# Kernel optimization log

Hardware: AMD Instinct MI355X
Metric: run time of the kernel (lower is better)

## Reference

```python
import jax, jax.numpy as jnp
import numpy as np

EPS = 1e-5

def _bn(x, gamma, beta):
    # x: [B, N, C]; training-mode BatchNorm1d over (B, N)
    mu = jnp.mean(x, axis=(0, 1))
    var = jnp.var(x, axis=(0, 1))
    return (x - mu) * jax.lax.rsqrt(var + EPS) * gamma + beta


def setup_inputs() -> dict:
    key = jax.random.key(0)
    ks = jax.random.split(key, 32)
    B, N = 16, 8192
    enc_dim, mem_dim = 1024, 1024
    feat_dim = enc_dim + mem_dim  # 2048
    n_points = 2048
    s = 0.02
    d = {
        'partial': jax.random.normal(ks[0], (B, N, 3), jnp.float32),
        # first_conv: Conv1d(3,128,1) + BN(128) + ReLU + Conv1d(128,256,1)
        'W1': jax.random.normal(ks[1], (128, 3), jnp.float32) * s,
        'b1': jnp.zeros((128,), jnp.float32),
        'g1': jnp.ones((128,), jnp.float32),
        'be1': jnp.zeros((128,), jnp.float32),
        'W2': jax.random.normal(ks[2], (256, 128), jnp.float32) * s,
        'b2': jnp.zeros((256,), jnp.float32),
        # second_conv: Conv1d(512,512,1) + BN(512) + ReLU + Conv1d(512,enc_dim,1)
        'W3': jax.random.normal(ks[3], (512, 512), jnp.float32) * s,
        'b3': jnp.zeros((512,), jnp.float32),
        'g2': jnp.ones((512,), jnp.float32),
        'be2': jnp.zeros((512,), jnp.float32),
        'W4': jax.random.normal(ks[4], (enc_dim, 512), jnp.float32) * s,
        'b4': jnp.zeros((enc_dim,), jnp.float32),
        # MemoryModule gates: Linear(enc_dim, mem_dim) x4 + memory param
        'Wf': jax.random.normal(ks[5], (mem_dim, enc_dim), jnp.float32) * s,
        'bf': jnp.zeros((mem_dim,), jnp.float32),
        'Wi': jax.random.normal(ks[6], (mem_dim, enc_dim), jnp.float32) * s,
        'bi': jnp.zeros((mem_dim,), jnp.float32),
        'Wo': jax.random.normal(ks[7], (mem_dim, enc_dim), jnp.float32) * s,
        'bo': jnp.zeros((mem_dim,), jnp.float32),
        'Wc': jax.random.normal(ks[8], (mem_dim, enc_dim), jnp.float32) * s,
        'bc': jnp.zeros((mem_dim,), jnp.float32),
        'mem': jax.random.normal(ks[9], (1, mem_dim), jnp.float32),
        # Decoder MLP: feat_dim->2048->2048->2048->3*n_points
        'D1w': jax.random.normal(ks[10], (2048, feat_dim), jnp.float32) * s,
        'D1b': jnp.zeros((2048,), jnp.float32),
        'D2w': jax.random.normal(ks[11], (2048, 2048), jnp.float32) * s,
        'D2b': jnp.zeros((2048,), jnp.float32),
        'D3w': jax.random.normal(ks[12], (2048, 2048), jnp.float32) * s,
        'D3b': jnp.zeros((2048,), jnp.float32),
        'D4w': jax.random.normal(ks[13], (3 * n_points, 2048), jnp.float32) * s,
        'D4b': jnp.zeros((3 * n_points,), jnp.float32),
    }
    return d


def reference(partial, W1, b1, g1, be1, W2, b2, W3, b3, g2, be2, W4, b4,
              Wf, bf, Wi, bi, Wo, bo, Wc, bc, mem,
              D1w, D1b, D2w, D2b, D3w, D3b, D4w, D4b):
    B, N, _ = partial.shape
    # --- Encoder first_conv (pointwise convs == per-point linear) ---
    f = jnp.einsum('bnc,dc->bnd', partial, W1) + b1          # [B,N,128]
    f = jax.nn.relu(_bn(f, g1, be1))
    f = jnp.einsum('bnc,dc->bnd', f, W2) + b2                # [B,N,256]
    fg = jnp.max(f, axis=1, keepdims=True)                   # [B,1,256]
    f = jnp.concatenate([jnp.broadcast_to(fg, (B, N, 256)), f], axis=-1)  # [B,N,512]
    # --- second_conv ---
    f = jnp.einsum('bnc,dc->bnd', f, W3) + b3                # [B,N,512]
    f = jax.nn.relu(_bn(f, g2, be2))
    f = jnp.einsum('bnc,dc->bnd', f, W4) + b4                # [B,N,enc_dim]
    feat_global = jnp.max(f, axis=1)                         # [B,enc_dim]
    # --- MemoryModule (flag=False: memory not updated) ---
    fgate = jax.nn.sigmoid(feat_global @ Wf.T + bf)
    igate = jax.nn.sigmoid(feat_global @ Wi.T + bi)
    ogate = jax.nn.sigmoid(feat_global @ Wo.T + bo)
    cand = jnp.tanh(feat_global @ Wc.T + bc)
    mem_b = jnp.broadcast_to(mem, fgate.shape)
    h = ogate * jnp.tanh(fgate * mem_b + igate * cand)       # [B,mem_dim]
    feat = jnp.concatenate([feat_global, h], axis=1)         # [B,feat_dim]
    # --- Decoder MLP ---
    z = jax.nn.relu(feat @ D1w.T + D1b)
    z = jax.nn.relu(z @ D2w.T + D2b)
    z = jax.nn.relu(z @ D3w.T + D3b)
    z = z @ D4w.T + D4b                                      # [B, 3*n_points]
    return z.reshape(B, -1, 3)
```

## Files before the change

kernel.cpp:

```cpp
#include <hip/hip_runtime.h>
#include <hip/hip_bf16.h>

typedef __bf16 v8bf __attribute__((ext_vector_type(8)));
typedef float  v4f  __attribute__((ext_vector_type(4)));

#define NPTS (16*8192)
#define RPB  8192

__device__ __forceinline__ unsigned fenc(float x){
    unsigned u = __float_as_uint(x);
    return (u & 0x80000000u) ? ~u : (u | 0x80000000u);
}
__device__ __forceinline__ float fdec(unsigned u){
    return __uint_as_float((u & 0x80000000u) ? (u ^ 0x80000000u) : ~u);
}

__device__ __forceinline__ v8bf bn_relu8(v8bf v, float4 s0, float4 s1, float4 h0, float4 h1){
    v8bf r;
    r[0] = (__bf16)fmaxf(fmaf((float)v[0], s0.x, h0.x), 0.f);
    r[1] = (__bf16)fmaxf(fmaf((float)v[1], s0.y, h0.y), 0.f);
    r[2] = (__bf16)fmaxf(fmaf((float)v[2], s0.z, h0.z), 0.f);
    r[3] = (__bf16)fmaxf(fmaf((float)v[3], s0.w, h0.w), 0.f);
    r[4] = (__bf16)fmaxf(fmaf((float)v[4], s1.x, h1.x), 0.f);
    r[5] = (__bf16)fmaxf(fmaf((float)v[5], s1.y, h1.y), 0.f);
    r[6] = (__bf16)fmaxf(fmaf((float)v[6], s1.z, h1.z), 0.f);
    r[7] = (__bf16)fmaxf(fmaf((float)v[7], s1.w, h1.w), 0.f);
    return r;
}

__global__ __launch_bounds__(256) void stats1_k(const float* __restrict__ P,
        const float* __restrict__ W1, const float* __restrict__ b1,
        float* __restrict__ gsum, float* __restrict__ gsumsq)
{
    int tid = threadIdx.x;
    int c = tid & 127, half = tid >> 7;
    float w0 = W1[c*3+0], w1 = W1[c*3+1], w2 = W1[c*3+2], bb = b1[c];
    float s = 0.f, s2 = 0.f;
    int base = blockIdx.x * 512 + half;
    for (int i = 0; i < 256; ++i) {
        int p = base + i*2;
        float x = P[p*3+0], y = P[p*3+1], z = P[p*3+2];
        float v = fmaf(w0,x, fmaf(w1,y, fmaf(w2,z, bb)));
        s += v; s2 = fmaf(v,v,s2);
    }
    __shared__ float ls[256], lq[256];
    ls[tid] = s; lq[tid] = s2;
    __syncthreads();
    if (half == 0) {
        atomicAdd(&gsum[c],   s  + ls[tid+128]);
        atomicAdd(&gsumsq[c], s2 + lq[tid+128]);
    }
}

__global__ void finalize_k(const float* __restrict__ gsum, const float* __restrict__ gsumsq,
        const float* __restrict__ gamma, const float* __restrict__ beta,
        float* __restrict__ scale, float* __restrict__ shift, int C, float invn)
{
    int c = blockIdx.x*blockDim.x + threadIdx.x;
    if (c >= C) return;
    float m   = gsum[c]*invn;
    float var = fmaxf(gsumsq[c]*invn - m*m, 0.f);
    float rs  = rsqrtf(var + 1e-5f);
    float sc  = gamma[c]*rs;
    scale[c] = sc;
    shift[c] = beta[c] - m*sc;
}

__global__ __launch_bounds__(256) void apply1_k(const float* __restrict__ P,
        const float* __restrict__ W1, const float* __restrict__ b1,
        const float* __restrict__ sc, const float* __restrict__ sh,
        __bf16* __restrict__ out)
{
    int tid = threadIdx.x;
    int c = tid & 127, ph = tid >> 7;
    float w0 = W1[c*3+0], w1 = W1[c*3+1], w2 = W1[c*3+2], bb = b1[c];
    float a = sc[c], b_ = sh[c];
    int base = blockIdx.x * 16 + ph;
    #pragma unroll
    for (int i = 0; i < 8; ++i) {
        int p = base + i*2;
        float x = P[p*3+0], y = P[p*3+1], z = P[p*3+2];
        float v = fmaf(w0,x, fmaf(w1,y, fmaf(w2,z, bb)));
        v = fmaxf(fmaf(v, a, b_), 0.f);
        out[(size_t)p*128 + c] = (__bf16)v;
    }
}

__global__ void cvt_k(const float* __restrict__ src, __bf16* __restrict__ dst,
                      int rows, int cols, int sstride, int coff)
{
    int i = blockIdx.x*256 + threadIdx.x;
    if (i >= rows*cols) return;
    int r = i / cols, c = i - r*cols;
    dst[i] = (__bf16)src[(size_t)r*sstride + coff + c];
}

template<bool STORE, bool DOMAX, bool STATS, bool BNA, int LOGNB>
__global__ __launch_bounds__(256, 2) void gemm_k(
        const __bf16* __restrict__ A, const __bf16* __restrict__ Bw,
        int K, int Nw,
        const float* __restrict__ bias, int bias_bstride,
        __bf16* __restrict__ Cout, unsigned* __restrict__ maxenc,
        float* __restrict__ gsum, float* __restrict__ gsq,
        const float* __restrict__ scA, const float* __restrict__ shA)
{
    __shared__ __bf16 As[128*64];
    __shared__ __bf16 Bs[256*64];
    __shared__ float lstat[2][2][256];

    const int tid  = threadIdx.x;
    const int lane = tid & 63;
    const int wave = tid >> 6;
    const int wr = wave >> 1, wc = wave & 1;
    const int nwg   = (int)gridDim.x;
    const int chunk = nwg >> 3;
    const int bi    = (int)blockIdx.x;
    const int li    = (bi & 7) * chunk + (bi >> 3);
    const int m0    = (li >> LOGNB) * 128;
    const int n0    = (li & ((1 << LOGNB) - 1)) * 256;
    const int srow = tid >> 3, sslot = tid & 7;

    v4f acc[4][8];
    #pragma unroll
    for (int i=0;i<4;i++)
      #pragma unroll
      for (int j=0;j<8;j++) acc[i][j] = (v4f)(0.0f);

    v8bf ra[4], rb[8];
    auto loadAB = [&](int kb){
        float4 s0{}, s1{}, h0{}, h1{};
        if constexpr (BNA) {
            int kk = kb + sslot*8;
            s0 = *(const float4*)(scA + kk);
            s1 = *(const float4*)(scA + kk + 4);
            h0 = *(const float4*)(shA + kk);
            h1 = *(const float4*)(shA + kk + 4);
        }
        #pragma unroll
        for (int i=0;i<4;i++){
            int r = i*32 + srow;
            v8bf v = *(const v8bf*)(A + (size_t)(m0+r)*K + kb + sslot*8);
            if constexpr (BNA) v = bn_relu8(v, s0, s1, h0, h1);
            ra[i] = v;
        }
        #pragma unroll
        for (int i=0;i<8;i++){
            int r = i*32 + srow;
            rb[i] = *(const v8bf*)(Bw + (size_t)(n0+r)*K + kb + sslot*8);
        }
    };

    loadAB(0);

    for (int k0 = 0; k0 < K; k0 += 64) {
        __syncthreads();
        #pragma unroll
        for (int i=0;i<4;i++){
            int r = i*32 + srow;
            int p = sslot ^ (r & 7);
            *(v8bf*)(&As[r*64 + p*8]) = ra[i];
        }
        #pragma unroll
        for (int i=0;i<8;i++){
            int r = i*32 + srow;
            int p = sslot ^ (r & 7);
            *(v8bf*)(&Bs[r*64 + p*8]) = rb[i];
        }
        __syncthreads();
        if (k0 + 64 < K) loadAB(k0 + 64);
        #pragma unroll
        for (int kk = 0; kk < 2; ++kk) {
            v8bf af[4], bfr[8];
            #pragma unroll
            for (int i=0;i<4;i++){
                int arow = wr*64 + i*16 + (lane & 15);
                int sg = kk*4 + (lane >> 4);
                af[i] = *(const v8bf*)(&As[arow*64 + ((sg ^ (arow & 7))<<3)]);
            }
            #pragma unroll
            for (int j=0;j<8;j++){
                int brow = wc*128 + j*16 + (lane & 15);
                int sg = kk*4 + (lane >> 4);
                bfr[j] = *(const v8bf*)(&Bs[brow*64 + ((sg ^ (brow & 7))<<3)]);
            }
            #pragma unroll
            for (int i=0;i<4;i++)
              #pragma unroll
              for (int j=0;j<8;j++)
                acc[i][j] = __builtin_amdgcn_mfma_f32_16x16x32_bf16(af[i], bfr[j], acc[i][j], 0,0,0);
        }
    }

    const int b = m0 / RPB;
    const float* brow_ = bias + (size_t)b * bias_bstride;
    float colmax[8], csum[8], csq[8];
    #pragma unroll
    for (int j=0;j<8;j++){ colmax[j] = -3.402823466e38f; csum[j]=0.f; csq[j]=0.f; }

    #pragma unroll
    for (int i=0;i<4;i++){
        int rbase = m0 + wr*64 + i*16 + ((lane>>4)<<2);
        #pragma unroll
        for (int j=0;j<8;j++){
            int col = n0 + wc*128 + j*16 + (lane & 15);
            float bv = brow_[col];
            #pragma unroll
            for (int q=0;q<4;q++){
                float v = acc[i][j][q] + bv;
                if constexpr (STORE) Cout[(size_t)(rbase+q)*Nw + col] = (__bf16)v;
                if constexpr (DOMAX) colmax[j] = fmaxf(colmax[j], v);
                if constexpr (STATS) { csum[j] += v; csq[j] = fmaf(v,v,csq[j]); }
            }
        }
    }
    if constexpr (DOMAX) {
        #pragma unroll
        for (int j=0;j<8;j++){
            float v = colmax[j];
            v = fmaxf(v, __shfl_xor(v, 16));
            v = fmaxf(v, __shfl_xor(v, 32));
            if (lane < 16) {
                int col = n0 + wc*128 + j*16 + lane;
                atomicMax(&maxenc[(size_t)b*Nw + col], fenc(v));
            }
        }
    }
    if constexpr (STATS) {
        #pragma unroll
        for (int j=0;j<8;j++){
            float s = csum[j], q = csq[j];
            s += __shfl_xor(s, 16); s += __shfl_xor(s, 32);
            q += __shfl_xor(q, 16); q += __shfl_xor(q, 32);
            if (lane < 16) {
                int c = wc*128 + j*16 + lane;
                lstat[0][wr][c] = s;
                lstat[1][wr][c] = q;
            }
        }
        __syncthreads();
        if (tid < 256) {
            float s = lstat[0][0][tid] + lstat[0][1][tid];
            float q = lstat[1][0][tid] + lstat[1][1][tid];
            atomicAdd(&gsum[n0 + tid], s);
            atomicAdd(&gsq [n0 + tid], q);
        }
    }
}

__global__ __launch_bounds__(256) void bias3_k(const unsigned* __restrict__ fge,
        const float* __restrict__ W3, const float* __restrict__ b3,
        float* __restrict__ bias3)
{
    int b = blockIdx.x, tid = threadIdx.x;
    __shared__ float fg[256];
    fg[tid] = fdec(fge[b*256 + tid]);
    __syncthreads();
    for (int d = tid; d < 512; d += 256) {
        const float* wrow = W3 + (size_t)d*512;
        float s = b3[d];
        for (int c = 0; c < 256; c += 4) {
            s = fmaf(fg[c+0], wrow[c+0], s);
            s = fmaf(fg[c+1], wrow[c+1], s);
            s = fmaf(fg[c+2], wrow[c+2], s);
            s = fmaf(fg[c+3], wrow[c+3], s);
        }
        bias3[b*512 + d] = s;
    }
}

__global__ void decode_k(const unsigned* __restrict__ enc, float* __restrict__ feat)
{
    int i = blockIdx.x*256 + threadIdx.x;
    int b = i >> 10, c = i & 1023;
    feat[(size_t)b*2048 + c] = fdec(enc[i]);
}

__global__ __launch_bounds__(256) void gates_k(
        const float* __restrict__ Wf, const float* __restrict__ bfv,
        const float* __restrict__ Wi, const float* __restrict__ biv,
        const float* __restrict__ Wo, const float* __restrict__ bov,
        const float* __restrict__ Wc, const float* __restrict__ bcv,
        const float* __restrict__ memv, float* __restrict__ feat)
{
    int tid = threadIdx.x;
    int b = tid & 15;
    int j = blockIdx.x*16 + (tid >> 4);
    const float* x  = feat + (size_t)b*2048;
    const float* rf = Wf + (size_t)j*1024;
    const float* ri = Wi + (size_t)j*1024;
    const float* ro = Wo + (size_t)j*1024;
    const float* rc = Wc + (size_t)j*1024;
    float sf = bfv[j], si = biv[j], so = bov[j], scn = bcv[j];
    for (int c = 0; c < 1024; c += 4) {
        float4 xv = *(const float4*)(x + c);
        float4 a  = *(const float4*)(rf + c);
        sf = fmaf(xv.x,a.x, fmaf(xv.y,a.y, fmaf(xv.z,a.z, fmaf(xv.w,a.w, sf))));
        float4 bq = *(const float4*)(ri + c);
        si = fmaf(xv.x,bq.x, fmaf(xv.y,bq.y, fmaf(xv.z,bq.z, fmaf(xv.w,bq.w, si))));
        float4 cq = *(const float4*)(ro + c);
        so = fmaf(xv.x,cq.x, fmaf(xv.y,cq.y, fmaf(xv.z,cq.z, fmaf(xv.w,cq.w, so))));
        float4 dq = *(const float4*)(rc + c);
        scn= fmaf(xv.x,dq.x, fmaf(xv.y,dq.y, fmaf(xv.z,dq.z, fmaf(xv.w,dq.w, scn))));
    }
    float fg = 1.f/(1.f + expf(-sf));
    float ig = 1.f/(1.f + expf(-si));
    float og = 1.f/(1.f + expf(-so));
    float cd = tanhf(scn);
    float h  = og * tanhf(fmaf(fg, memv[j], ig*cd));
    feat[(size_t)b*2048 + 1024 + j] = h;
}

template<bool RELU>
__global__ __launch_bounds__(256) void dec2_k(const float* __restrict__ in,
        const float* __restrict__ W, const float* __restrict__ bias,
        float* __restrict__ out, int N)
{
    __shared__ float xin[16*2048];
    int tid = threadIdx.x;
    for (int i = tid; i < 8192; i += 256)
        *(float4*)&xin[i*4] = *(const float4*)&in[i*4];
    __syncthreads();
    int lane = tid & 63, wv = tid >> 6;
    #pragma unroll
    for (int c = 0; c < 2; ++c) {
        int col = blockIdx.x*8 + wv*2 + c;
        const float* wrow = W + (size_t)col*2048;
        float s[16];
        #pragma unroll
        for (int b=0;b<16;b++) s[b]=0.f;
        #pragma unroll
        for (int it = 0; it < 8; ++it) {
            int k = it*256 + lane*4;
            float4 w4 = *(const float4*)(wrow + k);
            #pragma unroll
            for (int b=0;b<16;b++){
                const float* xb = &xin[b*2048 + k];
                s[b] = fmaf(w4.x, xb[0], fmaf(w4.y, xb[1], fmaf(w4.z, xb[2], fmaf(w4.w, xb[3], s[b]))));
            }
        }
        #pragma unroll
        for (int off=32; off; off>>=1){
            #pragma unroll
            for (int b=0;b<16;b++) s[b] += __shfl_xor(s[b], off);
        }
        if (lane == 0) {
            float bv = bias[col];
            #pragma unroll
            for (int b=0;b<16;b++){
                float v = s[b] + bv;
                if (RELU) v = fmaxf(v, 0.f);
                out[(size_t)b*N + col] = v;
            }
        }
    }
}

extern "C" void kernel_launch(void* const* d_in, const int* in_sizes, int n_in,
                              void* d_out, int out_size, void* d_ws, size_t ws_size,
                              hipStream_t stream)
{
    (void)in_sizes; (void)n_in; (void)out_size; (void)ws_size;
    const float* partial = (const float*)d_in[0];
    const float* W1 = (const float*)d_in[1];
    const float* b1 = (const float*)d_in[2];
    const float* g1 = (const float*)d_in[3];
    const float* be1= (const float*)d_in[4];
    const float* W2 = (const float*)d_in[5];
    const float* b2 = (const float*)d_in[6];
    const float* W3 = (const float*)d_in[7];
    const float* b3 = (const float*)d_in[8];
    const float* g2 = (const float*)d_in[9];
    const float* be2= (const float*)d_in[10];
    const float* W4 = (const float*)d_in[11];
    const float* b4 = (const float*)d_in[12];
    const float* Wf = (const float*)d_in[13];
    const float* bfv= (const float*)d_in[14];
    const float* Wi = (const float*)d_in[15];
    const float* biv= (const float*)d_in[16];
    const float* Wo = (const float*)d_in[17];
    const float* bov= (const float*)d_in[18];
    const float* Wc = (const float*)d_in[19];
    const float* bcv= (const float*)d_in[20];
    const float* memv=(const float*)d_in[21];
    const float* D1w= (const float*)d_in[22];
    const float* D1b= (const float*)d_in[23];
    const float* D2w= (const float*)d_in[24];
    const float* D2b= (const float*)d_in[25];
    const float* D3w= (const float*)d_in[26];
    const float* D3b= (const float*)d_in[27];
    const float* D4w= (const float*)d_in[28];
    const float* D4b= (const float*)d_in[29];

    char* w = (char*)d_ws;
    size_t off = 0;
    auto alloc = [&](size_t bytes) -> void* {
        void* p = w + off; off += (bytes + 255) & ~(size_t)255; return p;
    };
    __bf16* y1bn = (__bf16*)alloc((size_t)NPTS*128*2);
    __bf16* f2   = (__bf16*)alloc((size_t)NPTS*256*2);
    __bf16* y3   = (__bf16*)alloc((size_t)NPTS*512*2);
    __bf16* W2b  = (__bf16*)alloc(256*128*2);
    __bf16* W3bb = (__bf16*)alloc(512*256*2);
    __bf16* W4b  = (__bf16*)alloc(1024*512*2);
    char* accbase = (char*)(w + off);
    float* gsum1    = (float*)alloc(128*4);
    float* gsumsq1  = (float*)alloc(128*4);
    float* gsum3    = (float*)alloc(512*4);
    float* gsumsq3  = (float*)alloc(512*4);
    unsigned* fg_enc    = (unsigned*)alloc(16*256*4);
    unsigned* featg_enc = (unsigned*)alloc(16*1024*4);
    size_t accbytes = (size_t)((w + off) - accbase);
    float* scale1 = (float*)alloc(128*4);
    float* shift1 = (float*)alloc(128*4);
    float* scale3 = (float*)alloc(512*4);
    float* shift3 = (float*)alloc(512*4);
    float* bias3  = (float*)alloc(16*512*4);
    float* feat   = (float*)alloc(16*2048*4);
    float* z1     = (float*)alloc(16*2048*4);
    float* z2     = (float*)alloc(16*2048*4);
    float* z3     = (float*)alloc(16*2048*4);

    hipMemsetAsync(accbase, 0, accbytes, stream);

    cvt_k<<<dim3(128), 256, 0, stream>>>(W2, W2b, 256, 128, 128, 0);
    cvt_k<<<dim3(512), 256, 0, stream>>>(W3, W3bb, 512, 256, 512, 256);
    cvt_k<<<dim3(2048),256, 0, stream>>>(W4, W4b, 1024, 512, 512, 0);

    stats1_k<<<dim3(256), 256, 0, stream>>>(partial, W1, b1, gsum1, gsumsq1);
    finalize_k<<<dim3(1), 128, 0, stream>>>(gsum1, gsumsq1, g1, be1, scale1, shift1, 128, 1.f/NPTS);
    apply1_k<<<dim3(8192), 256, 0, stream>>>(partial, W1, b1, scale1, shift1, y1bn);

    gemm_k<true,true,false,false,0><<<dim3(1024), 256, 0, stream>>>(
        y1bn, W2b, 128, 256, b2, 0, f2, fg_enc, nullptr, nullptr, nullptr, nullptr);

    bias3_k<<<dim3(16), 256, 0, stream>>>(fg_enc, W3, b3, bias3);

    gemm_k<true,false,true,false,1><<<dim3(2048), 256, 0, stream>>>(
        f2, W3bb, 256, 512, bias3, 512, y3, nullptr, gsum3, gsumsq3, nullptr, nullptr);

    finalize_k<<<dim3(2), 256, 0, stream>>>(gsum3, gsumsq3, g2, be2, scale3, shift3, 512, 1.f/NPTS);

    gemm_k<false,true,false,true,2><<<dim3(4096), 256, 0, stream>>>(
        y3, W4b, 512, 1024, b4, 0, nullptr, featg_enc, nullptr, nullptr, scale3, shift3);

    decode_k<<<dim3(64), 256, 0, stream>>>(featg_enc, feat);
    gates_k<<<dim3(64), 256, 0, stream>>>(Wf,bfv, Wi,biv, Wo,bov, Wc,bcv, memv, feat);

    dec2_k<true ><<<dim3(256), 256, 0, stream>>>(feat, D1w, D1b, z1, 2048);
    dec2_k<true ><<<dim3(256), 256, 0, stream>>>(z1,   D2w, D2b, z2, 2048);
    dec2_k<true ><<<dim3(256), 256, 0, stream>>>(z2,   D3w, D3b, z3, 2048);
    dec2_k<false><<<dim3(768), 256, 0, stream>>>(z3,   D4w, D4b, (float*)d_out, 6144);
}
```

Baseline: 502.8 us.

## Stage GEMM tiles and decoder inputs via direct global-to-LDS loads

Replaces register-staged global loads followed by LDS stores with buffer global_load_lds (direct-to-LDS) for the weight tile B, for the A tile when no BN is fused, and for the decoder input vector copy. The swizzled layout is reproduced by permuting the global source column per lane. This drops VGPR pressure and the register round trip, but loses the register prefetch overlap: B is now loaded after the barrier in the same iteration, with no double buffering, so load latency may become exposed.

```diff
diff --git a/kernel.cpp b/kernel.cpp
--- a/kernel.cpp
+++ b/kernel.cpp
@@ -6,6 +6,10 @@
 
 #define NPTS (16*8192)
 #define RPB  8192
+
+#define GLOAD_LDS16(g, l) __builtin_amdgcn_global_load_lds( \
+    (const __attribute__((address_space(1))) void*)(g), \
+    (__attribute__((address_space(3))) void*)(l), 16, 0, 0)
 
 __device__ __forceinline__ unsigned fenc(float x){
     unsigned u = __float_as_uint(x);
@@ -119,6 +123,8 @@
     const int m0    = (li >> LOGNB) * 128;
     const int n0    = (li & ((1 << LOGNB) - 1)) * 256;
     const int srow = tid >> 3, sslot = tid & 7;
+    const int lrow  = lane >> 3;
+    const int swz   = ((lane & 7) ^ lrow) * 8;
 
     v4f acc[4][8];
     #pragma unroll
@@ -126,48 +132,51 @@
       #pragma unroll
       for (int j=0;j<8;j++) acc[i][j] = (v4f)(0.0f);
 
-    v8bf ra[4], rb[8];
-    auto loadAB = [&](int kb){
-        float4 s0{}, s1{}, h0{}, h1{};
-        if constexpr (BNA) {
-            int kk = kb + sslot*8;
-            s0 = *(const float4*)(scA + kk);
-            s1 = *(const float4*)(scA + kk + 4);
-            h0 = *(const float4*)(shA + kk);
-            h1 = *(const float4*)(shA + kk + 4);
-        }
+    v8bf ra[4];
+    auto loadA_bn = [&](int kb){
+        int kk = kb + sslot*8;
+        float4 s0 = *(const float4*)(scA + kk);
+        float4 s1 = *(const float4*)(scA + kk + 4);
+        float4 h0 = *(const float4*)(shA + kk);
+        float4 h1 = *(const float4*)(shA + kk + 4);
         #pragma unroll
         for (int i=0;i<4;i++){
             int r = i*32 + srow;
             v8bf v = *(const v8bf*)(A + (size_t)(m0+r)*K + kb + sslot*8);
-            if constexpr (BNA) v = bn_relu8(v, s0, s1, h0, h1);
-            ra[i] = v;
-        }
-        #pragma unroll
-        for (int i=0;i<8;i++){
-            int r = i*32 + srow;
-            rb[i] = *(const v8bf*)(Bw + (size_t)(n0+r)*K + kb + sslot*8);
+            ra[i] = bn_relu8(v, s0, s1, h0, h1);
         }
     };
-
-    loadAB(0);
+    auto stageB = [&](int kb){
+        #pragma unroll
+        for (int j=0;j<8;j++){
+            int r0 = (wave*8 + j)*8;
+            GLOAD_LDS16(Bw + (size_t)(n0 + r0 + lrow)*K + kb + swz, &Bs[r0*64]);
+        }
+    };
+    auto stageA = [&](int kb){
+        #pragma unroll
+        for (int j=0;j<4;j++){
+            int r0 = (wave*4 + j)*8;
+            GLOAD_LDS16(A + (size_t)(m0 + r0 + lrow)*K + kb + swz, &As[r0*64]);
+        }
+    };
+
+    if constexpr (BNA) loadA_bn(0);
 
     for (int k0 = 0; k0 < K; k0 += 64) {
         __syncthreads();
-        #pragma unroll
-        for (int i=0;i<4;i++){
-            int r = i*32 + srow;
-            int p = sslot ^ (r & 7);
-            *(v8bf*)(&As[r*64 + p*8]) = ra[i];
-        }
-        #pragma unroll
-        for (int i=0;i<8;i++){
-            int r = i*32 + srow;
-            int p = sslot ^ (r & 7);
-            *(v8bf*)(&Bs[r*64 + p*8]) = rb[i];
+        stageB(k0);
+        if constexpr (BNA) {
+            #pragma unroll
+            for (int i=0;i<4;i++){
+                int r = i*32 + srow;
+                *(v8bf*)(&As[r*64 + ((sslot ^ (r & 7))<<3)]) = ra[i];
+            }
+        } else {
+            stageA(k0);
         }
         __syncthreads();
-        if (k0 + 64 < K) loadAB(k0 + 64);
+        if constexpr (BNA) { if (k0 + 64 < K) loadA_bn(k0 + 64); }
         #pragma unroll
         for (int kk = 0; kk < 2; ++kk) {
             v8bf af[4], bfr[8];
@@ -317,10 +326,13 @@
 {
     __shared__ float xin[16*2048];
     int tid = threadIdx.x;
-    for (int i = tid; i < 8192; i += 256)
-        *(float4*)&xin[i*4] = *(const float4*)&in[i*4];
+    int lane = tid & 63, wv = tid >> 6;
+    #pragma unroll
+    for (int j = 0; j < 32; ++j) {
+        int blk = wv*32 + j;
+        GLOAD_LDS16(in + blk*256 + lane*4, &xin[blk*256]);
+    }
     __syncthreads();
-    int lane = tid & 63, wv = tid >> 6;
     #pragma unroll
     for (int c = 0; c < 2; ++c) {
         int col = blockIdx.x*8 + wv*2 + c;
```

Result: faster. 478.6 us, median of 2 (-4.8%).
